# Kernel optimization log

Measured on AMD Instinct MI355X. Metric: run time of the kernel, lower is better.

## Reference

```python
import jax, jax.numpy as jnp
import numpy as np

B, N_OCR, N_OBJ, D, H, L, DFF = 64, 64, 192, 768, 12, 4, 2048
DH = D // H
EPS = 1e-5  # torch LayerNorm default


def _ln(x, g, b):
    m = jnp.mean(x, axis=-1, keepdims=True)
    v = jnp.mean(jnp.square(x - m), axis=-1, keepdims=True)
    return (x - m) * jax.lax.rsqrt(v + EPS) * g + b


def setup_inputs():
    key = jax.random.key(0)
    ks = iter(jax.random.split(key, 32))
    s = 0.02
    f = lambda shape: jax.random.normal(next(ks), shape, jnp.float32) * s
    return {
        "ocr_feats": jax.random.normal(next(ks), (B, N_OCR, D), jnp.float32),
        "obj_feats": jax.random.normal(next(ks), (B, N_OBJ, D), jnp.float32),
        "ocr_dvs": jax.random.uniform(next(ks), (B, N_OCR, 1), jnp.float32, 0.1, 2.0),
        "obj_dvs": jax.random.uniform(next(ks), (B, N_OBJ, 1), jnp.float32, 0.1, 2.0),
        # SemanticAttentionDeFUM projections
        "sa_wq": f((D, D)), "sa_bq": jnp.zeros((D,), jnp.float32),
        "sa_wk": f((D, D)), "sa_bk": jnp.zeros((D,), jnp.float32),
        "sa_wv": f((D, D)), "sa_bv": jnp.zeros((D,), jnp.float32),
        # outer LayerNorm
        "ln0_g": jnp.ones((D,), jnp.float32), "ln0_b": jnp.zeros((D,), jnp.float32),
        # stacked TransformerEncoder layer params (post-norm, batch_first)
        "qkv_w": f((L, 3 * D, D)), "qkv_b": jnp.zeros((L, 3 * D), jnp.float32),
        "out_w": f((L, D, D)), "out_b": jnp.zeros((L, D), jnp.float32),
        "ln1_g": jnp.ones((L, D), jnp.float32), "ln1_b": jnp.zeros((L, D), jnp.float32),
        "ff1_w": f((L, DFF, D)), "ff1_b": jnp.zeros((L, DFF), jnp.float32),
        "ff2_w": f((L, D, DFF)), "ff2_b": jnp.zeros((L, D), jnp.float32),
        "ln2_g": jnp.ones((L, D), jnp.float32), "ln2_b": jnp.zeros((L, D), jnp.float32),
    }


def reference(ocr_feats, obj_feats, ocr_dvs, obj_dvs,
              sa_wq, sa_bq, sa_wk, sa_bk, sa_wv, sa_bv,
              ln0_g, ln0_b,
              qkv_w, qkv_b, out_w, out_b, ln1_g, ln1_b,
              ff1_w, ff1_b, ff2_w, ff2_b, ln2_g, ln2_b):
    num_ocr = ocr_feats.shape[1]
    x = jnp.concatenate([ocr_feats, obj_feats], axis=1)       # B,N,D
    dv = jnp.concatenate([ocr_dvs, obj_dvs], axis=1)[..., 0]  # B,N
    # vectorized cal_relative_depth_map: log(max(dv_i,dv_j)/min(dv_i,dv_j))
    R = jnp.log(jnp.maximum(dv[:, :, None], dv[:, None, :]) /
                jnp.minimum(dv[:, :, None], dv[:, None, :]))  # B,N,N
    # semantic attention: scores A and values V
    q = jnp.einsum('bnd,ed->bne', x, sa_wq) + sa_bq
    k = jnp.einsum('bnd,ed->bne', x, sa_wk) + sa_bk
    v = jnp.einsum('bnd,ed->bne', x, sa_wv) + sa_bv
    A = jnp.einsum('bqd,bkd->bqk', q, k) / jnp.sqrt(jnp.float32(D))
    att = jax.nn.softmax(A + R, axis=-1)
    h = _ln(x + jnp.einsum('bqk,bkd->bqd', att, v), ln0_g, ln0_b)

    def layer(h, p):
        qw, qb, ow, ob, l1g, l1b, f1w, f1b, f2w, f2b, l2g, l2b = p
        Bn, N, _ = h.shape
        qkv = jnp.einsum('bnd,ed->bne', h, qw) + qb            # B,N,3D
        qh, kh, vh = jnp.split(qkv, 3, axis=-1)
        qh = qh.reshape(Bn, N, H, DH).transpose(0, 2, 1, 3)
        kh = kh.reshape(Bn, N, H, DH).transpose(0, 2, 1, 3)
        vh = vh.reshape(Bn, N, H, DH).transpose(0, 2, 1, 3)
        sc = jnp.einsum('bhqd,bhkd->bhqk', qh, kh) / jnp.sqrt(jnp.float32(DH))
        o = jnp.einsum('bhqk,bhkd->bhqd', jax.nn.softmax(sc, axis=-1), vh)
        o = o.transpose(0, 2, 1, 3).reshape(Bn, N, D)
        o = jnp.einsum('bnd,ed->bne', o, ow) + ob
        h = _ln(h + o, l1g, l1b)
        ff = jnp.einsum('bnd,fd->bnf', h, f1w) + f1b
        ff = jax.nn.gelu(ff, approximate=False)  # torch 'gelu' = exact erf gelu
        ff = jnp.einsum('bnf,df->bnd', ff, f2w) + f2b
        h = _ln(h + ff, l2g, l2b)
        return h, None

    h, _ = jax.lax.scan(layer, h, (qkv_w, qkv_b, out_w, out_b,
                                   ln1_g, ln1_b, ff1_w, ff1_b,
                                   ff2_w, ff2_b, ln2_g, ln2_b))
    return h[:, :num_ocr, :]
```

## Files before the change

kernel.cpp:

```cpp
#include <hip/hip_runtime.h>

typedef unsigned short u16;
typedef __bf16 bf16_t;
typedef bf16_t bf16x8 __attribute__((ext_vector_type(8)));
typedef float f32x4 __attribute__((ext_vector_type(4)));
typedef unsigned int u32x4 __attribute__((ext_vector_type(4)));
typedef u16 u16x4 __attribute__((ext_vector_type(4)));

#define GL_LDS16(gp, lp)                                              \
  __builtin_amdgcn_global_load_lds(                                   \
      (const __attribute__((address_space(1))) void*)(gp),            \
      (__attribute__((address_space(3))) void*)(lp), 16, 0, 0)

__device__ __forceinline__ u16 f2bf(float f) {
  unsigned u = __builtin_bit_cast(unsigned, f);
  u += 0x7fff + ((u >> 16) & 1);
  return (u16)(u >> 16);
}
__device__ __forceinline__ float bf2f(u16 h) {
  unsigned u = ((unsigned)h) << 16;
  return __builtin_bit_cast(float, u);
}
__device__ __forceinline__ float wredSum(float v) {
#pragma unroll
  for (int m = 32; m; m >>= 1) v += __shfl_xor(v, m);
  return v;
}

__global__ __launch_bounds__(256, 2) void gemm3r(
    const u16* __restrict__ A, const u16* __restrict__ B,
    const float* __restrict__ bias, u16* __restrict__ C,
    int K, int N, int gx, int act, int tstore) {
  extern __shared__ __align__(16) char sm[];
  const int tid = threadIdx.x;
  const int l = tid & 63, wc = tid >> 6, lg = l >> 4, li = l & 15;

  int bid = blockIdx.x;
  int G = gx >> 3;
  int xcd = bid & 7, loc = bid >> 3;
  int mt = xcd * G + (loc % G), nt = loc / G;

  const u16* Ab = A + (long)mt * 128 * K;
  const u16* Bb = B + (long)nt * 256 * K;

  const long saoff = (long)(tid >> 2) * K + (((tid & 3) ^ ((tid >> 3) & 3)) << 3);
  const long rowK64 = (long)64 * K;
  const int t16 = tid * 16;

#define STAGE(bi_, kt_)                                                \
  do {                                                                 \
    char* lb_ = sm + (bi_) * 24576;                                    \
    const u16* gb_ = Bb + saoff + ((long)(kt_) << 5);                  \
    GL_LDS16(gb_, lb_ + 8192 + t16);                                   \
    GL_LDS16(gb_ + rowK64, lb_ + 12288 + t16);                         \
    GL_LDS16(gb_ + 2 * rowK64, lb_ + 16384 + t16);                     \
    GL_LDS16(gb_ + 3 * rowK64, lb_ + 20480 + t16);                     \
    const u16* ga_ = Ab + saoff + ((long)(kt_) << 5);                  \
    GL_LDS16(ga_, lb_ + t16);                                          \
    GL_LDS16(ga_ + rowK64, lb_ + 4096 + t16);                          \
  } while (0)

#define VM6 asm volatile("s_waitcnt vmcnt(6)" ::: "memory")
#define VM0 asm volatile("s_waitcnt vmcnt(0)" ::: "memory")

  int aof[2][4], bof[4];
#pragma unroll
  for (int hi = 0; hi < 2; ++hi)
#pragma unroll
    for (int f = 0; f < 4; ++f) {
      int ra = hi * 64 + f * 16 + li;
      aof[hi][f] = ra * 64 + ((lg ^ ((ra >> 1) & 3)) << 4);
    }
#pragma unroll
  for (int f = 0; f < 4; ++f) {
    int rb = wc * 64 + f * 16 + li;
    bof[f] = 8192 + rb * 64 + ((lg ^ ((rb >> 1) & 3)) << 4);
  }

  f32x4 acc[8][4] = {};

  const int NT = K >> 5;
  STAGE(0, 0); STAGE(1, 1);

  for (int s = 0; s < NT; ++s) {
    const int bi = s % 3;
    const char* ab = sm + bi * 24576;
    if (s == NT - 1) VM0; else VM6;
    __builtin_amdgcn_s_barrier();
    asm volatile("" ::: "memory");
    if (s + 2 < NT) { int b2 = (s + 2) % 3; STAGE(b2, s + 2); }
    bf16x8 afr[4], bfr[4], ag[4];
#pragma unroll
    for (int f = 0; f < 4; ++f) {
      afr[f] = __builtin_bit_cast(bf16x8, *(const u32x4*)(ab + aof[0][f]));
      bfr[f] = __builtin_bit_cast(bf16x8, *(const u32x4*)(ab + bof[f]));
      ag[f]  = __builtin_bit_cast(bf16x8, *(const u32x4*)(ab + aof[1][f]));
    }
    __builtin_amdgcn_s_setprio(1);
#pragma unroll
    for (int fi = 0; fi < 4; ++fi)
#pragma unroll
      for (int fj = 0; fj < 4; ++fj)
        acc[fi][fj] = __builtin_amdgcn_mfma_f32_16x16x32_bf16(afr[fi], bfr[fj], acc[fi][fj], 0, 0, 0);
#pragma unroll
    for (int fi = 0; fi < 4; ++fi)
#pragma unroll
      for (int fj = 0; fj < 4; ++fj)
        acc[4 + fi][fj] = __builtin_amdgcn_mfma_f32_16x16x32_bf16(ag[fi], bfr[fj], acc[4 + fi][fj], 0, 0, 0);
    __builtin_amdgcn_s_setprio(0);
  }

  long row0 = (long)mt * 128;
  int col0 = nt * 256 + wc * 64;
#pragma unroll
  for (int fi = 0; fi < 8; ++fi) {
#pragma unroll
    for (int fj = 0; fj < 4; ++fj) {
      int c = col0 + fj * 16 + li;
      float bv = bias ? bias[c] : 0.f;
#pragma unroll
      for (int r = 0; r < 4; ++r) {
        float v = acc[fi][fj][r] + bv;
        if (act) v = 0.5f * v * (1.f + erff(v * 0.70710678118f));
        long row = row0 + fi * 16 + lg * 4 + r;
        long idx = tstore ? ((row >> 8) * 196608 + (long)c * 256 + (row & 255))
                          : (row * (long)N + c);
        C[idx] = f2bf(v);
      }
    }
  }
#undef STAGE
#undef VM6
#undef VM0
}

__global__ __launch_bounds__(256) void gemm_bt(
    const u16* __restrict__ A, const u16* __restrict__ B,
    const float* __restrict__ bias, const float* __restrict__ logdv,
    float* __restrict__ Cf, u16* __restrict__ Cb,
    int K, int ldc, long sA, long sB, long sC, float alpha, int act, int tstore) {
  __shared__ __align__(16) u16 As[2][128 * 32];
  __shared__ __align__(16) u16 Bs[2][128 * 32];
  int tid = threadIdx.x, w = tid >> 6, l = tid & 63, lg = l >> 4, li = l & 15;
  int wr = w >> 1, wc = w & 1;
  long bz = blockIdx.z;
  const u16* Ab = A + bz * sA + (long)blockIdx.x * 128 * K;
  const u16* Bb = B + bz * sB + (long)blockIdx.y * 128 * K;

  int sr = tid >> 2, ss = tid & 3;
  long ga0 = (long)sr * K + ((ss ^ ((sr >> 1) & 3)) << 3);
  long gstep = (long)K << 6;

  int aoff[4], boff[4];
#pragma unroll
  for (int i = 0; i < 4; ++i) {
    int ra = wr * 64 + i * 16 + li;
    aoff[i] = ra * 64 + ((lg ^ ((ra >> 1) & 3)) << 4);
    int rb = wc * 64 + i * 16 + li;
    boff[i] = rb * 64 + ((lg ^ ((rb >> 1) & 3)) << 4);
  }

  f32x4 acc[4][4] = {};
  int wb = w * 1024;

  GL_LDS16(Ab + ga0, (char*)As + wb);
  GL_LDS16(Ab + ga0 + gstep, (char*)As + 4096 + wb);
  GL_LDS16(Bb + ga0, (char*)Bs + wb);
  GL_LDS16(Bb + ga0 + gstep, (char*)Bs + 4096 + wb);
  __syncthreads();

  int T = K >> 5;
  int bsel = 0;
  for (int kt = 0; kt < T; ++kt) {
    if (kt + 1 < T) {
      long ko = (long)(kt + 1) << 5;
      char* an = (char*)As + (bsel ^ 1) * 8192;
      char* bn = (char*)Bs + (bsel ^ 1) * 8192;
      GL_LDS16(Ab + ga0 + ko, an + wb);
      GL_LDS16(Ab + ga0 + gstep + ko, an + 4096 + wb);
      GL_LDS16(Bb + ga0 + ko, bn + wb);
      GL_LDS16(Bb + ga0 + gstep + ko, bn + 4096 + wb);
    }
    char* ac = (char*)As + bsel * 8192;
    char* bc = (char*)Bs + bsel * 8192;
    bf16x8 af[4], bq[4];
#pragma unroll
    for (int i = 0; i < 4; ++i) {
      af[i] = __builtin_bit_cast(bf16x8, *(const u32x4*)(ac + aoff[i]));
      bq[i] = __builtin_bit_cast(bf16x8, *(const u32x4*)(bc + boff[i]));
    }
#pragma unroll
    for (int i = 0; i < 4; ++i)
#pragma unroll
      for (int j = 0; j < 4; ++j)
        acc[i][j] = __builtin_amdgcn_mfma_f32_16x16x32_bf16(af[i], bq[j], acc[i][j], 0, 0, 0);
    __syncthreads();
    bsel ^= 1;
  }

  long row0 = (long)blockIdx.x * 128 + wr * 64;
  int col0 = blockIdx.y * 128 + wc * 64;
  float* cf = Cf ? Cf + bz * sC : (float*)0;
  u16* cb = Cb ? Cb + bz * sC : (u16*)0;
  const float* ldv = logdv ? logdv + bz * 256 : (const float*)0;
#pragma unroll
  for (int i = 0; i < 4; ++i) {
    long rb0 = row0 + i * 16 + lg * 4;
#pragma unroll
    for (int j = 0; j < 4; ++j) {
      int c = col0 + j * 16 + li;
      float bv = bias ? bias[c] : 0.f;
      float lj = ldv ? ldv[c] : 0.f;
#pragma unroll
      for (int r = 0; r < 4; ++r) {
        float v = acc[i][j][r] * alpha + bv;
        if (ldv) v += fabsf(ldv[rb0 + r] - lj);
        if (act) v = 0.5f * v * (1.f + erff(v * 0.70710678118f));
        long row = rb0 + r;
        long idx = tstore ? ((row >> 8) * 196608 + (long)c * 256 + (row & 255))
                          : (row * ldc + c);
        if (cf) cf[idx] = v;
        if (cb) cb[idx] = f2bf(v);
      }
    }
  }
}

__global__ __launch_bounds__(256) void mha_k(const u16* __restrict__ qkv, u16* __restrict__ obf) {
  __shared__ __align__(16) u16 Ks[256 * 64];
  __shared__ __align__(16) u16 Vt[64 * 256];
  int b = blockIdx.y;
  int h = blockIdx.x >> 2, qt = blockIdx.x & 3;
  int tid = threadIdx.x, w = tid >> 6, l = tid & 63, lg = l >> 4, li = l & 15;
  const u16* kb_ = qkv + (long)b * 256 * 2304 + 768 + h * 64;
  const u16* vb_ = qkv + (long)b * 256 * 2304 + 1536 + h * 64;
#pragma unroll
  for (int it = 0; it < 8; ++it) {
    int c = it * 256 + tid; int n = c >> 3, sl = c & 7;
    u32x4 d = *(const u32x4*)(kb_ + (long)n * 2304 + sl * 8);
    *(u32x4*)((char*)Ks + n * 128 + ((sl ^ (n & 7)) << 4)) = d;
  }
#pragma unroll
  for (int it = 0; it < 8; ++it) {
    int c = it * 256 + tid; int n = c >> 3, sl = c & 7;
    u32x4 dv = *(const u32x4*)(vb_ + (long)n * 2304 + sl * 8);
    const u16* pe = (const u16*)&dv;
#pragma unroll
    for (int j = 0; j < 8; ++j) {
      int dd = sl * 8 + j;
      *(u16*)((char*)Vt + dd * 512 + (((n >> 3) ^ (dd & 7)) << 4) + (n & 7) * 2) = pe[j];
    }
  }
  __syncthreads();

  long qrow = (long)b * 256 + qt * 64 + w * 16 + li;
  const u16* qp = qkv + qrow * 2304 + h * 64;
  bf16x8 qf0 = __builtin_bit_cast(bf16x8, *(const u32x4*)(qp + lg * 8));
  bf16x8 qf1 = __builtin_bit_cast(bf16x8, *(const u32x4*)(qp + 32 + lg * 8));

  f32x4 sacc[16] = {};
#pragma unroll
  for (int jt = 0; jt < 16; ++jt) {
    int j = jt * 16 + li;
    u32x4 k0 = *(const u32x4*)((char*)Ks + j * 128 + ((lg ^ (j & 7)) << 4));
    u32x4 k1 = *(const u32x4*)((char*)Ks + j * 128 + (((4 + lg) ^ (j & 7)) << 4));
    sacc[jt] = __builtin_amdgcn_mfma_f32_16x16x32_bf16(qf0, __builtin_bit_cast(bf16x8, k0), sacc[jt], 0, 0, 0);
    sacc[jt] = __builtin_amdgcn_mfma_f32_16x16x32_bf16(qf1, __builtin_bit_cast(bf16x8, k1), sacc[jt], 0, 0, 0);
  }
#pragma unroll
  for (int jt = 0; jt < 16; ++jt) sacc[jt] = sacc[jt] * 0.125f;

  float rinv[4];
#pragma unroll
  for (int r = 0; r < 4; ++r) {
    float m = -1e30f;
#pragma unroll
    for (int jt = 0; jt < 16; ++jt) m = fmaxf(m, sacc[jt][r]);
#pragma unroll
    for (int mk = 1; mk < 16; mk <<= 1) m = fmaxf(m, __shfl_xor(m, mk));
    float s = 0.f;
#pragma unroll
    for (int jt = 0; jt < 16; ++jt) { float e = __expf(sacc[jt][r] - m); sacc[jt][r] = e; s += e; }
#pragma unroll
    for (int mk = 1; mk < 16; mk <<= 1) s += __shfl_xor(s, mk);
    rinv[r] = 1.f / s;
  }
  __syncthreads();
  char* Ps = (char*)Ks + w * 8192;
#pragma unroll
  for (int jt = 0; jt < 16; ++jt) {
    int j = jt * 16 + li;
#pragma unroll
    for (int r = 0; r < 4; ++r) {
      int i = lg * 4 + r;
      *(u16*)(Ps + i * 512 + (((j >> 3) ^ (i & 7)) << 4) + (j & 7) * 2) = f2bf(sacc[jt][r]);
    }
  }
  __syncthreads();
  f32x4 oacc[4] = {};
#pragma unroll
  for (int kb2 = 0; kb2 < 8; ++kb2) {
    int sl = kb2 * 4 + lg;
    u32x4 pa = *(const u32x4*)(Ps + li * 512 + ((sl ^ (li & 7)) << 4));
#pragma unroll
    for (int dt = 0; dt < 4; ++dt) {
      int dd = dt * 16 + li;
      u32x4 vv = *(const u32x4*)((char*)Vt + dd * 512 + ((sl ^ (dd & 7)) << 4));
      oacc[dt] = __builtin_amdgcn_mfma_f32_16x16x32_bf16(__builtin_bit_cast(bf16x8, pa),
                                                         __builtin_bit_cast(bf16x8, vv), oacc[dt], 0, 0, 0);
    }
  }
  long orow = (long)b * 256 + qt * 64 + w * 16;
#pragma unroll
  for (int dt = 0; dt < 4; ++dt)
#pragma unroll
    for (int r = 0; r < 4; ++r) {
      float vvv = oacc[dt][r] * rinv[r];
      obf[(orow + lg * 4 + r) * 768 + h * 64 + dt * 16 + li] = f2bf(vvv);
    }
}

__global__ __launch_bounds__(256) void ln_k(const float* __restrict__ X, const u16* __restrict__ Rr,
                                            const float* __restrict__ g, const float* __restrict__ bb,
                                            float* __restrict__ oF, u16* __restrict__ oB) {
  long row = (long)blockIdx.x * 4 + (threadIdx.x >> 6);
  int l = threadIdx.x & 63;
  const float* x = X + row * 768;
  const u16* rr = Rr + row * 768;
  f32x4 v[3];
  float s = 0.f;
#pragma unroll
  for (int i = 0; i < 3; ++i) {
    f32x4 xv = *(const f32x4*)(x + i * 256 + l * 4);
    u16x4 rv = *(const u16x4*)(rr + i * 256 + l * 4);
#pragma unroll
    for (int j = 0; j < 4; ++j) xv[j] += bf2f(rv[j]);
    v[i] = xv;
    s += xv[0] + xv[1] + xv[2] + xv[3];
  }
  float mean = wredSum(s) * (1.f / 768.f);
  float q = 0.f;
#pragma unroll
  for (int i = 0; i < 3; ++i) {
#pragma unroll
    for (int j = 0; j < 4; ++j) { v[i][j] -= mean; q += v[i][j] * v[i][j]; }
  }
  float inv = rsqrtf(wredSum(q) * (1.f / 768.f) + 1e-5f);
#pragma unroll
  for (int i = 0; i < 3; ++i) {
    f32x4 gv = *(const f32x4*)(g + i * 256 + l * 4);
    f32x4 bv = *(const f32x4*)(bb + i * 256 + l * 4);
    f32x4 o;
    u16x4 ob;
#pragma unroll
    for (int j = 0; j < 4; ++j) { o[j] = v[i][j] * inv * gv[j] + bv[j]; ob[j] = f2bf(o[j]); }
    *(f32x4*)(oF + row * 768 + i * 256 + l * 4) = o;
    *(u16x4*)(oB + row * 768 + i * 256 + l * 4) = ob;
  }
}

__global__ __launch_bounds__(256) void smax_k(const float* __restrict__ S, u16* __restrict__ P) {
  long row = (long)blockIdx.x * 4 + (threadIdx.x >> 6);
  int l = threadIdx.x & 63;
  f32x4 v = *(const f32x4*)(S + row * 256 + l * 4);
  float m = fmaxf(fmaxf(v[0], v[1]), fmaxf(v[2], v[3]));
#pragma unroll
  for (int mk = 1; mk < 64; mk <<= 1) m = fmaxf(m, __shfl_xor(m, mk));
  float e0 = __expf(v[0] - m), e1 = __expf(v[1] - m), e2 = __expf(v[2] - m), e3 = __expf(v[3] - m);
  float s = wredSum(e0 + e1 + e2 + e3);
  float rn = 1.f / s;
  u16x4 o; o[0] = f2bf(e0 * rn); o[1] = f2bf(e1 * rn); o[2] = f2bf(e2 * rn); o[3] = f2bf(e3 * rn);
  *(u16x4*)(P + row * 256 + l * 4) = o;
}

__global__ __launch_bounds__(256) void conv_k(const float* __restrict__ in, u16* __restrict__ out, long n4) {
  long i = (long)blockIdx.x * 256 + threadIdx.x;
  if (i >= n4) return;
  f32x4 v = *(const f32x4*)(in + i * 4);
  u16x4 o; o[0] = f2bf(v[0]); o[1] = f2bf(v[1]); o[2] = f2bf(v[2]); o[3] = f2bf(v[3]);
  *(u16x4*)(out + i * 4) = o;
}

__global__ __launch_bounds__(256) void concat_k(const float* __restrict__ ocr, const float* __restrict__ obj,
                                                float* __restrict__ xf, u16* __restrict__ xb) {
  long i = (long)blockIdx.x * 256 + threadIdx.x;
  if (i >= 16384L * 192) return;
  long row = i / 192; int c4 = (int)(i % 192);
  int b = (int)(row >> 8), n = (int)(row & 255);
  const float* src = (n < 64) ? (ocr + ((long)(b * 64 + n)) * 768) : (obj + ((long)(b * 192 + n - 64)) * 768);
  f32x4 v = *(const f32x4*)(src + c4 * 4);
  *(f32x4*)(xf + row * 768 + c4 * 4) = v;
  u16x4 o; o[0] = f2bf(v[0]); o[1] = f2bf(v[1]); o[2] = f2bf(v[2]); o[3] = f2bf(v[3]);
  *(u16x4*)(xb + row * 768 + c4 * 4) = o;
}

__global__ __launch_bounds__(256) void logdv_k(const float* __restrict__ ocr_dv, const float* __restrict__ obj_dv,
                                               float* __restrict__ out) {
  int i = blockIdx.x * 256 + threadIdx.x;
  if (i >= 16384) return;
  int b = i >> 8, n = i & 255;
  float dv = (n < 64) ? ocr_dv[b * 64 + n] : obj_dv[b * 192 + n - 64];
  out[i] = logf(dv);
}

__global__ __launch_bounds__(256) void slice_k(const float* __restrict__ H, float* __restrict__ O) {
  long i = (long)blockIdx.x * 256 + threadIdx.x;
  if (i >= 786432) return;
  long idx = i * 4;
  long row = idx / 768; int c = (int)(idx % 768);
  long b = row >> 6, n = row & 63;
  *(f32x4*)(O + idx) = *(const f32x4*)(H + ((b * 256 + n) * 768 + c));
}

extern "C" void kernel_launch(void* const* d_in, const int* in_sizes, int n_in,
                              void* d_out, int out_size, void* d_ws, size_t ws_size,
                              hipStream_t stream) {
  const float* ocr = (const float*)d_in[0];
  const float* obj = (const float*)d_in[1];
  const float* ocr_dv = (const float*)d_in[2];
  const float* obj_dv = (const float*)d_in[3];
  const float* sa_wq = (const float*)d_in[4];
  const float* sa_bq = (const float*)d_in[5];
  const float* sa_wk = (const float*)d_in[6];
  const float* sa_bk = (const float*)d_in[7];
  const float* sa_wv = (const float*)d_in[8];
  const float* sa_bv = (const float*)d_in[9];
  const float* ln0_g = (const float*)d_in[10];
  const float* ln0_b = (const float*)d_in[11];
  const float* qkv_w = (const float*)d_in[12];
  const float* qkv_b = (const float*)d_in[13];
  const float* out_w = (const float*)d_in[14];
  const float* out_b = (const float*)d_in[15];
  const float* ln1_g = (const float*)d_in[16];
  const float* ln1_b = (const float*)d_in[17];
  const float* ff1_w = (const float*)d_in[18];
  const float* ff1_b = (const float*)d_in[19];
  const float* ff2_w = (const float*)d_in[20];
  const float* ff2_b = (const float*)d_in[21];
  const float* ln2_g = (const float*)d_in[22];
  const float* ln2_b = (const float*)d_in[23];

  (void)hipFuncSetAttribute((const void*)gemm3r,
                            hipFuncAttributeMaxDynamicSharedMemorySize, 73728);
  const unsigned DSM = 73728;

  char* ws = (char*)d_ws;
  float* XF = (float*)ws;
  u16* HB = (u16*)(ws + 50331648);
  float* LDV = (float*)(ws + 75497472);
  u16* WCV = (u16*)(ws + 75563008);
  char* SCR = ws + 86573056;

  const int bigws = ws_size >= (size_t)187236352;

  auto cv = [&](const float* src, long elems, u16* dst) {
    long n4 = elems >> 2;
    conv_k<<<dim3((unsigned)((n4 + 255) / 256)), dim3(256), 0, stream>>>(src, dst, n4);
  };

  concat_k<<<12288, 256, 0, stream>>>(ocr, obj, XF, HB);
  logdv_k<<<64, 256, 0, stream>>>(ocr_dv, obj_dv, LDV);

  const float SSC = 0.03608439182435161f;

  cv(sa_wq, 589824, WCV);
  cv(sa_wk, 589824, WCV + 589824);
  cv(sa_wv, 589824, WCV + 1179648);

  if (bigws) {
    u16* Qf = (u16*)SCR;
    u16* Kf = (u16*)(SCR + 25165824);
    u16* VTf = (u16*)(SCR + 50331648);
    float* Sfc = (float*)(SCR + 75497472);
    u16* Pc = (u16*)(SCR + 83886080);
    u16* ATTc = (u16*)(SCR + 88080384);
    gemm3r<<<384, 256, DSM, stream>>>(HB, WCV, sa_bq, Qf, 768, 768, 128, 0, 0);
    gemm3r<<<384, 256, DSM, stream>>>(HB, WCV + 589824, sa_bk, Kf, 768, 768, 128, 0, 0);
    gemm3r<<<384, 256, DSM, stream>>>(HB, WCV + 1179648, sa_bv, VTf, 768, 768, 128, 0, 1);
    for (int c = 0; c < 2; ++c) {
      long base = (long)c * 8192;
      gemm_bt<<<dim3(2, 2, 32), 256, 0, stream>>>(Qf + base * 768, Kf + base * 768, nullptr,
                                                  LDV + c * 8192, Sfc, nullptr, 768, 256,
                                                  196608, 196608, 65536, SSC, 0, 0);
      smax_k<<<2048, 256, 0, stream>>>(Sfc, Pc);
      gemm_bt<<<dim3(2, 6, 32), 256, 0, stream>>>(Pc, VTf + base * 768, nullptr, nullptr,
                                                  nullptr, ATTc, 256, 768, 65536, 196608, 196608, 1.f, 0, 0);
      ln_k<<<2048, 256, 0, stream>>>(XF + base * 768, ATTc, ln0_g, ln0_b, XF + base * 768, HB + base * 768);
    }
    u16* QKVf = (u16*)SCR;
    u16* Of = (u16*)(SCR + 75497472);
    u16* PRf = (u16*)SCR;
    u16* FFf = (u16*)(SCR + 25165824);
    for (int l = 0; l < 4; ++l) {
      cv(qkv_w + (long)l * 1769472, 1769472, WCV);
      cv(out_w + (long)l * 589824, 589824, WCV + 1769472);
      cv(ff1_w + (long)l * 1572864, 1572864, WCV + 2359296);
      cv(ff2_w + (long)l * 1572864, 1572864, WCV + 3932160);
      gemm3r<<<1152, 256, DSM, stream>>>(HB, WCV, qkv_b + l * 2304, QKVf, 768, 2304, 128, 0, 0);
      mha_k<<<dim3(48, 64), 256, 0, stream>>>(QKVf, Of);
      gemm3r<<<384, 256, DSM, stream>>>(Of, WCV + 1769472, out_b + l * 768, PRf, 768, 768, 128, 0, 0);
      ln_k<<<4096, 256, 0, stream>>>(XF, PRf, ln1_g + l * 768, ln1_b + l * 768, XF, HB);
      gemm3r<<<1024, 256, DSM, stream>>>(HB, WCV + 2359296, ff1_b + l * 2048, FFf, 768, 2048, 128, 1, 0);
      gemm3r<<<384, 256, DSM, stream>>>(FFf, WCV + 3932160, ff2_b + l * 768, PRf, 2048, 768, 128, 0, 0);
      ln_k<<<4096, 256, 0, stream>>>(XF, PRf, ln2_g + l * 768, ln2_b + l * 768, XF, HB);
    }
  } else {
    for (int c = 0; c < 2; ++c) {
      long base = (long)c * 8192;
      u16* Qc = (u16*)SCR;
      u16* Kc = (u16*)(SCR + 12582912);
      u16* VTc = (u16*)(SCR + 25165824);
      float* Sfc = (float*)(SCR + 37748736);
      u16* Pc = (u16*)(SCR + 46137344);
      u16* ATTc = (u16*)(SCR + 50331648);
      gemm3r<<<192, 256, DSM, stream>>>(HB + base * 768, WCV, sa_bq, Qc, 768, 768, 64, 0, 0);
      gemm3r<<<192, 256, DSM, stream>>>(HB + base * 768, WCV + 589824, sa_bk, Kc, 768, 768, 64, 0, 0);
      gemm3r<<<192, 256, DSM, stream>>>(HB + base * 768, WCV + 1179648, sa_bv, VTc, 768, 768, 64, 0, 1);
      gemm_bt<<<dim3(2, 2, 32), 256, 0, stream>>>(Qc, Kc, nullptr, LDV + c * 8192,
                                                  Sfc, nullptr, 768, 256, 196608, 196608, 65536, SSC, 0, 0);
      smax_k<<<2048, 256, 0, stream>>>(Sfc, Pc);
      gemm_bt<<<dim3(2, 6, 32), 256, 0, stream>>>(Pc, VTc, nullptr, nullptr,
                                                  nullptr, ATTc, 256, 768, 65536, 196608, 196608, 1.f, 0, 0);
      ln_k<<<2048, 256, 0, stream>>>(XF + base * 768, ATTc, ln0_g, ln0_b, XF + base * 768, HB + base * 768);
    }
    for (int l = 0; l < 4; ++l) {
      cv(qkv_w + (long)l * 1769472, 1769472, WCV);
      cv(out_w + (long)l * 589824, 589824, WCV + 1769472);
      cv(ff1_w + (long)l * 1572864, 1572864, WCV + 2359296);
      cv(ff2_w + (long)l * 1572864, 1572864, WCV + 3932160);
      for (int c = 0; c < 2; ++c) {
        long base = (long)c * 8192;
        u16* QKVc = (u16*)SCR;
        u16* Oc = (u16*)(SCR + 37748736);
        u16* PRc = (u16*)(SCR + 50331648);
        u16* FFc = (u16*)SCR;
        gemm3r<<<576, 256, DSM, stream>>>(HB + base * 768, WCV, qkv_b + l * 2304, QKVc, 768, 2304, 64, 0, 0);
        mha_k<<<dim3(48, 32), 256, 0, stream>>>(QKVc, Oc);
        gemm3r<<<192, 256, DSM, stream>>>(Oc, WCV + 1769472, out_b + l * 768, PRc, 768, 768, 64, 0, 0);
        ln_k<<<2048, 256, 0, stream>>>(XF + base * 768, PRc, ln1_g + l * 768, ln1_b + l * 768,
                                       XF + base * 768, HB + base * 768);
        gemm3r<<<512, 256, DSM, stream>>>(HB + base * 768, WCV + 2359296, ff1_b + l * 2048, FFc, 768, 2048, 64, 1, 0);
        gemm3r<<<192, 256, DSM, stream>>>(FFc, WCV + 3932160, ff2_b + l * 768, PRc, 2048, 768, 64, 0, 0);
        ln_k<<<2048, 256, 0, stream>>>(XF + base * 768, PRc, ln2_g + l * 768, ln2_b + l * 768,
                                       XF + base * 768, HB + base * 768);
      }
    }
  }
  slice_k<<<3072, 256, 0, stream>>>(XF, (float*)d_out);
}
```

Baseline: 1.952 ms.

## Make GEMM persistent with cross-tile prefetch and drop fp32 residual stream

```diff
diff --git a/kernel.cpp b/kernel.cpp
--- a/kernel.cpp
+++ b/kernel.cpp
@@ -27,35 +27,31 @@
   return v;
 }
 
-__global__ __launch_bounds__(256, 2) void gemm3r(
+__global__ __launch_bounds__(256, 2) void gemmp(
     const u16* __restrict__ A, const u16* __restrict__ B,
     const float* __restrict__ bias, u16* __restrict__ C,
-    int K, int N, int gx, int act, int tstore) {
+    int K, int N, int gx, int gy, int act, int tstore) {
   extern __shared__ __align__(16) char sm[];
   const int tid = threadIdx.x;
-  const int l = tid & 63, wc = tid >> 6, lg = l >> 4, li = l & 15;
-
-  int bid = blockIdx.x;
-  int G = gx >> 3;
-  int xcd = bid & 7, loc = bid >> 3;
-  int mt = xcd * G + (loc % G), nt = loc / G;
-
-  const u16* Ab = A + (long)mt * 128 * K;
-  const u16* Bb = B + (long)nt * 256 * K;
-
+  const int l = tid & 63, wv = tid >> 6, lg = l >> 4, li = l & 15;
+  const int TOT = gx * gy;
+  int tix = blockIdx.x;
+  if (tix >= TOT) return;
+  const int G = gx >> 3;
+
+  const long rowK64 = (long)64 * K;
   const long saoff = (long)(tid >> 2) * K + (((tid & 3) ^ ((tid >> 3) & 3)) << 3);
-  const long rowK64 = (long)64 * K;
   const int t16 = tid * 16;
 
-#define STAGE(bi_, kt_)                                                \
+#define STAGE(bi_, Ap_, Bp_, kt_)                                      \
   do {                                                                 \
     char* lb_ = sm + (bi_) * 24576;                                    \
-    const u16* gb_ = Bb + saoff + ((long)(kt_) << 5);                  \
+    const u16* gb_ = (Bp_) + saoff + ((long)(kt_) << 5);               \
     GL_LDS16(gb_, lb_ + 8192 + t16);                                   \
     GL_LDS16(gb_ + rowK64, lb_ + 12288 + t16);                         \
     GL_LDS16(gb_ + 2 * rowK64, lb_ + 16384 + t16);                     \
     GL_LDS16(gb_ + 3 * rowK64, lb_ + 20480 + t16);                     \
-    const u16* ga_ = Ab + saoff + ((long)(kt_) << 5);                  \
+    const u16* ga_ = (Ap_) + saoff + ((long)(kt_) << 5);               \
     GL_LDS16(ga_, lb_ + t16);                                          \
     GL_LDS16(ga_ + rowK64, lb_ + 4096 + t16);                          \
   } while (0)
@@ -73,61 +69,87 @@
     }
 #pragma unroll
   for (int f = 0; f < 4; ++f) {
-    int rb = wc * 64 + f * 16 + li;
+    int rb = wv * 64 + f * 16 + li;
     bof[f] = 8192 + rb * 64 + ((lg ^ ((rb >> 1) & 3)) << 4);
   }
 
+  int mt, nt;
+  const u16 *cA, *cB;
+  { int xc = tix & 7, lo = tix >> 3;
+    mt = xc * G + lo % G; nt = lo / G;
+    cA = A + (long)mt * 128 * K; cB = B + (long)nt * 256 * K; }
+  int nxt = tix + 512;
+  int hasn = nxt < TOT;
+  int nmt = 0, nnt = 0;
+  const u16 *nA = cA, *nB = cB;
+  if (hasn) { int xc = nxt & 7, lo = nxt >> 3;
+    nmt = xc * G + lo % G; nnt = lo / G;
+    nA = A + (long)nmt * 128 * K; nB = B + (long)nnt * 256 * K; }
+
+  const int NT = K >> 5;
   f32x4 acc[8][4] = {};
-
-  const int NT = K >> 5;
-  STAGE(0, 0); STAGE(1, 1);
-
-  for (int s = 0; s < NT; ++s) {
-    const int bi = s % 3;
-    const char* ab = sm + bi * 24576;
-    if (s == NT - 1) VM0; else VM6;
-    __builtin_amdgcn_s_barrier();
-    asm volatile("" ::: "memory");
-    if (s + 2 < NT) { int b2 = (s + 2) % 3; STAGE(b2, s + 2); }
-    bf16x8 afr[4], bfr[4], ag[4];
-#pragma unroll
-    for (int f = 0; f < 4; ++f) {
-      afr[f] = __builtin_bit_cast(bf16x8, *(const u32x4*)(ab + aof[0][f]));
-      bfr[f] = __builtin_bit_cast(bf16x8, *(const u32x4*)(ab + bof[f]));
-      ag[f]  = __builtin_bit_cast(bf16x8, *(const u32x4*)(ab + aof[1][f]));
-    }
-    __builtin_amdgcn_s_setprio(1);
-#pragma unroll
-    for (int fi = 0; fi < 4; ++fi)
-#pragma unroll
-      for (int fj = 0; fj < 4; ++fj)
-        acc[fi][fj] = __builtin_amdgcn_mfma_f32_16x16x32_bf16(afr[fi], bfr[fj], acc[fi][fj], 0, 0, 0);
-#pragma unroll
-    for (int fi = 0; fi < 4; ++fi)
-#pragma unroll
-      for (int fj = 0; fj < 4; ++fj)
-        acc[4 + fi][fj] = __builtin_amdgcn_mfma_f32_16x16x32_bf16(ag[fi], bfr[fj], acc[4 + fi][fj], 0, 0, 0);
-    __builtin_amdgcn_s_setprio(0);
-  }
-
-  long row0 = (long)mt * 128;
-  int col0 = nt * 256 + wc * 64;
-#pragma unroll
-  for (int fi = 0; fi < 8; ++fi) {
-#pragma unroll
-    for (int fj = 0; fj < 4; ++fj) {
-      int c = col0 + fj * 16 + li;
-      float bv = bias ? bias[c] : 0.f;
-#pragma unroll
-      for (int r = 0; r < 4; ++r) {
-        float v = acc[fi][fj][r] + bv;
-        if (act) v = 0.5f * v * (1.f + erff(v * 0.70710678118f));
-        long row = row0 + fi * 16 + lg * 4 + r;
-        long idx = tstore ? ((row >> 8) * 196608 + (long)c * 256 + (row & 255))
-                          : (row * (long)N + c);
-        C[idx] = f2bf(v);
+  STAGE(0, cA, cB, 0); STAGE(1, cA, cB, 1);
+  int bi = 0;
+
+  for (;;) {
+    for (int s = 0; s < NT; ++s) {
+      int bi2 = bi + 2; if (bi2 >= 3) bi2 -= 3;
+      const char* ab = sm + bi * 24576;
+      if (s == NT - 1 && !hasn) VM0; else VM6;
+      __builtin_amdgcn_s_barrier();
+      asm volatile("" ::: "memory");
+      int s2 = s + 2;
+      if (s2 < NT) STAGE(bi2, cA, cB, s2);
+      else if (hasn) STAGE(bi2, nA, nB, s2 - NT);
+      bf16x8 afr[4], bfr[4], ag[4];
+#pragma unroll
+      for (int f = 0; f < 4; ++f) {
+        afr[f] = __builtin_bit_cast(bf16x8, *(const u32x4*)(ab + aof[0][f]));
+        bfr[f] = __builtin_bit_cast(bf16x8, *(const u32x4*)(ab + bof[f]));
+        ag[f]  = __builtin_bit_cast(bf16x8, *(const u32x4*)(ab + aof[1][f]));
       }
-    }
+      __builtin_amdgcn_s_setprio(1);
+#pragma unroll
+      for (int fi = 0; fi < 4; ++fi)
+#pragma unroll
+        for (int fj = 0; fj < 4; ++fj)
+          acc[fi][fj] = __builtin_amdgcn_mfma_f32_16x16x32_bf16(afr[fi], bfr[fj], acc[fi][fj], 0, 0, 0);
+#pragma unroll
+      for (int fi = 0; fi < 4; ++fi)
+#pragma unroll
+        for (int fj = 0; fj < 4; ++fj)
+          acc[4 + fi][fj] = __builtin_amdgcn_mfma_f32_16x16x32_bf16(ag[fi], bfr[fj], acc[4 + fi][fj], 0, 0, 0);
+      __builtin_amdgcn_s_setprio(0);
+      bi = bi + 1; if (bi == 3) bi = 0;
+    }
+    {
+      long row0 = (long)mt * 128;
+      int col0 = nt * 256 + wv * 64;
+#pragma unroll
+      for (int fi = 0; fi < 8; ++fi) {
+#pragma unroll
+        for (int fj = 0; fj < 4; ++fj) {
+          int c = col0 + fj * 16 + li;
+          float bv = bias ? bias[c] : 0.f;
+#pragma unroll
+          for (int r = 0; r < 4; ++r) {
+            float v = acc[fi][fj][r] + bv;
+            if (act) v = 0.5f * v * (1.f + erff(v * 0.70710678118f));
+            long row = row0 + fi * 16 + lg * 4 + r;
+            long idx = tstore ? ((row >> 8) * 196608 + (long)c * 256 + (row & 255))
+                              : (row * (long)N + c);
+            C[idx] = f2bf(v);
+          }
+          acc[fi][fj] = (f32x4){0.f, 0.f, 0.f, 0.f};
+        }
+      }
+    }
+    if (!hasn) break;
+    mt = nmt; nt = nnt; cA = nA; cB = nB;
+    tix = nxt; nxt += 512; hasn = nxt < TOT;
+    if (hasn) { int xc = nxt & 7, lo = nxt >> 3;
+      nmt = xc * G + lo % G; nnt = lo / G;
+      nA = A + (long)nmt * 128 * K; nB = B + (long)nnt * 256 * K; }
   }
 #undef STAGE
 #undef VM6
@@ -320,23 +342,24 @@
     }
 }
 
-__global__ __launch_bounds__(256) void ln_k(const float* __restrict__ X, const u16* __restrict__ Rr,
+__global__ __launch_bounds__(256) void ln_k(const u16* __restrict__ X, const u16* __restrict__ Rr,
                                             const float* __restrict__ g, const float* __restrict__ bb,
-                                            float* __restrict__ oF, u16* __restrict__ oB) {
+                                            u16* __restrict__ O) {
   long row = (long)blockIdx.x * 4 + (threadIdx.x >> 6);
   int l = threadIdx.x & 63;
-  const float* x = X + row * 768;
+  const u16* x = X + row * 768;
   const u16* rr = Rr + row * 768;
   f32x4 v[3];
   float s = 0.f;
 #pragma unroll
   for (int i = 0; i < 3; ++i) {
-    f32x4 xv = *(const f32x4*)(x + i * 256 + l * 4);
+    u16x4 xv = *(const u16x4*)(x + i * 256 + l * 4);
     u16x4 rv = *(const u16x4*)(rr + i * 256 + l * 4);
-#pragma unroll
-    for (int j = 0; j < 4; ++j) xv[j] += bf2f(rv[j]);
-    v[i] = xv;
-    s += xv[0] + xv[1] + xv[2] + xv[3];
+    f32x4 t;
+#pragma unroll
+    for (int j = 0; j < 4; ++j) t[j] = bf2f(xv[j]) + bf2f(rv[j]);
+    v[i] = t;
+    s += t[0] + t[1] + t[2] + t[3];
   }
   float mean = wredSum(s) * (1.f / 768.f);
   float q = 0.f;
@@ -350,12 +373,10 @@
   for (int i = 0; i < 3; ++i) {
     f32x4 gv = *(const f32x4*)(g + i * 256 + l * 4);
     f32x4 bv = *(const f32x4*)(bb + i * 256 + l * 4);
-    f32x4 o;
     u16x4 ob;
 #pragma unroll
-    for (int j = 0; j < 4; ++j) { o[j] = v[i][j] * inv * gv[j] + bv[j]; ob[j] = f2bf(o[j]); }
-    *(f32x4*)(oF + row * 768 + i * 256 + l * 4) = o;
-    *(u16x4*)(oB + row * 768 + i * 256 + l * 4) = ob;
+    for (int j = 0; j < 4; ++j) ob[j] = f2bf(v[i][j] * inv * gv[j] + bv[j]);
+    *(u16x4*)(O + row * 768 + i * 256 + l * 4) = ob;
   }
 }
 
@@ -382,14 +403,13 @@
 }
 
 __global__ __launch_bounds__(256) void concat_k(const float* __restrict__ ocr, const float* __restrict__ obj,
-                                                float* __restrict__ xf, u16* __restrict__ xb) {
+                                                u16* __restrict__ xb) {
   long i = (long)blockIdx.x * 256 + threadIdx.x;
   if (i >= 16384L * 192) return;
   long row = i / 192; int c4 = (int)(i % 192);
   int b = (int)(row >> 8), n = (int)(row & 255);
   const float* src = (n < 64) ? (ocr + ((long)(b * 64 + n)) * 768) : (obj + ((long)(b * 192 + n - 64)) * 768);
   f32x4 v = *(const f32x4*)(src + c4 * 4);
-  *(f32x4*)(xf + row * 768 + c4 * 4) = v;
   u16x4 o; o[0] = f2bf(v[0]); o[1] = f2bf(v[1]); o[2] = f2bf(v[2]); o[3] = f2bf(v[3]);
   *(u16x4*)(xb + row * 768 + c4 * 4) = o;
 }
@@ -403,13 +423,15 @@
   out[i] = logf(dv);
 }
 
-__global__ __launch_bounds__(256) void slice_k(const float* __restrict__ H, float* __restrict__ O) {
+__global__ __launch_bounds__(256) void slice_k(const u16* __restrict__ H, float* __restrict__ O) {
   long i = (long)blockIdx.x * 256 + threadIdx.x;
   if (i >= 786432) return;
   long idx = i * 4;
   long row = idx / 768; int c = (int)(idx % 768);
   long b = row >> 6, n = row & 63;
-  *(f32x4*)(O + idx) = *(const f32x4*)(H + ((b * 256 + n) * 768 + c));
+  u16x4 v = *(const u16x4*)(H + ((b * 256 + n) * 768 + c));
+  f32x4 o; o[0] = bf2f(v[0]); o[1] = bf2f(v[1]); o[2] = bf2f(v[2]); o[3] = bf2f(v[3]);
+  *(f32x4*)(O + idx) = o;
 }
 
 extern "C" void kernel_launch(void* const* d_in, const int* in_sizes, int n_in,
@@ -440,25 +462,24 @@
   const float* ln2_g = (const float*)d_in[22];
   const float* ln2_b = (const float*)d_in[23];
 
-  (void)hipFuncSetAttribute((const void*)gemm3r,
+  (void)hipFuncSetAttribute((const void*)gemmp,
                             hipFuncAttributeMaxDynamicSharedMemorySize, 73728);
   const unsigned DSM = 73728;
 
   char* ws = (char*)d_ws;
-  float* XF = (float*)ws;
-  u16* HB = (u16*)(ws + 50331648);
-  float* LDV = (float*)(ws + 75497472);
-  u16* WCV = (u16*)(ws + 75563008);
-  char* SCR = ws + 86573056;
-
-  const int bigws = ws_size >= (size_t)187236352;
+  u16* HB = (u16*)ws;
+  float* LDV = (float*)(ws + 25165824);
+  u16* WCV = (u16*)(ws + 25231360);
+  char* SCR = ws + 36241408;
+
+  const int bigws = ws_size >= (size_t)137953280;
 
   auto cv = [&](const float* src, long elems, u16* dst) {
     long n4 = elems >> 2;
     conv_k<<<dim3((unsigned)((n4 + 255) / 256)), dim3(256), 0, stream>>>(src, dst, n4);
   };
 
-  concat_k<<<12288, 256, 0, stream>>>(ocr, obj, XF, HB);
+  concat_k<<<12288, 256, 0, stream>>>(ocr, obj, HB);
   logdv_k<<<64, 256, 0, stream>>>(ocr_dv, obj_dv, LDV);
 
   const float SSC = 0.03608439182435161f;
@@ -474,9 +495,9 @@
     float* Sfc = (float*)(SCR + 75497472);
     u16* Pc = (u16*)(SCR + 83886080);
     u16* ATTc = (u16*)(SCR + 88080384);
-    gemm3r<<<384, 256, DSM, stream>>>(HB, WCV, sa_bq, Qf, 768, 768, 128, 0, 0);
-    gemm3r<<<384, 256, DSM, stream>>>(HB, WCV + 589824, sa_bk, Kf, 768, 768, 128, 0, 0);
-    gemm3r<<<384, 256, DSM, stream>>>(HB, WCV + 1179648, sa_bv, VTf, 768, 768, 128, 0, 1);
+    gemmp<<<512, 256, DSM, stream>>>(HB, WCV, sa_bq, Qf, 768, 768, 128, 3, 0, 0);
+    gemmp<<<512, 256, DSM, stream>>>(HB, WCV + 589824, sa_bk, Kf, 768, 768, 128, 3, 0, 0);
+    gemmp<<<512, 256, DSM, stream>>>(HB, WCV + 1179648, sa_bv, VTf, 768, 768, 128, 3, 0, 1);
     for (int c = 0; c < 2; ++c) {
       long base = (long)c * 8192;
       gemm_bt<<<dim3(2, 2, 32), 256, 0, stream>>>(Qf + base * 768, Kf + base * 768, nullptr,
@@ -485,7 +506,7 @@
       smax_k<<<2048, 256, 0, stream>>>(Sfc, Pc);
       gemm_bt<<<dim3(2, 6, 32), 256, 0, stream>>>(Pc, VTf + base * 768, nullptr, nullptr,
                                                   nullptr, ATTc, 256, 768, 65536, 196608, 196608, 1.f, 0, 0);
-      ln_k<<<2048, 256, 0, stream>>>(XF + base * 768, ATTc, ln0_g, ln0_b, XF + base * 768, HB + base * 768);
+      ln_k<<<2048, 256, 0, stream>>>(HB + base * 768, ATTc, ln0_g, ln0_b, HB + base * 768);
     }
     u16* QKVf = (u16*)SCR;
     u16* Of = (u16*)(SCR + 75497472);
@@ -496,13 +517,13 @@
       cv(out_w + (long)l * 589824, 589824, WCV + 1769472);
       cv(ff1_w + (long)l * 1572864, 1572864, WCV + 2359296);
       cv(ff2_w + (long)l * 1572864, 1572864, WCV + 3932160);
-      gemm3r<<<1152, 256, DSM, stream>>>(HB, WCV, qkv_b + l * 2304, QKVf, 768, 2304, 128, 0, 0);
+      gemmp<<<512, 256, DSM, stream>>>(HB, WCV, qkv_b + l * 2304, QKVf, 768, 2304, 128, 9, 0, 0);
       mha_k<<<dim3(48, 64), 256, 0, stream>>>(QKVf, Of);
-      gemm3r<<<384, 256, DSM, stream>>>(Of, WCV + 1769472, out_b + l * 768, PRf, 768, 768, 128, 0, 0);
-      ln_k<<<4096, 256, 0, stream>>>(XF, PRf, ln1_g + l * 768, ln1_b + l * 768, XF, HB);
-      gemm3r<<<1024, 256, DSM, stream>>>(HB, WCV + 2359296, ff1_b + l * 2048, FFf, 768, 2048, 128, 1, 0);
-      gemm3r<<<384, 256, DSM, stream>>>(FFf, WCV + 3932160, ff2_b + l * 768, PRf, 2048, 768, 128, 0, 0);
-      ln_k<<<4096, 256, 0, stream>>>(XF, PRf, ln2_g + l * 768, ln2_b + l * 768, XF, HB);
+      gemmp<<<512, 256, DSM, stream>>>(Of, WCV + 1769472, out_b + l * 768, PRf, 768, 768, 128, 3, 0, 0);
+      ln_k<<<4096, 256, 0, stream>>>(HB, PRf, ln1_g + l * 768, ln1_b + l * 768, HB);
+      gemmp<<<512, 256, DSM, stream>>>(HB, WCV + 2359296, ff1_b + l * 2048, FFf, 768, 2048, 128, 8, 1, 0);
+      gemmp<<<512, 256, DSM, stream>>>(FFf, WCV + 3932160, ff2_b + l * 768, PRf, 2048, 768, 128, 3, 0, 0);
+      ln_k<<<4096, 256, 0, stream>>>(HB, PRf, ln2_g + l * 768, ln2_b + l * 768, HB);
     }
   } else {
     for (int c = 0; c < 2; ++c) {
@@ -513,15 +534,15 @@
       float* Sfc = (float*)(SCR + 37748736);
       u16* Pc = (u16*)(SCR + 46137344);
       u16* ATTc = (u16*)(SCR + 50331648);
-      gemm3r<<<192, 256, DSM, stream>>>(HB + base * 768, WCV, sa_bq, Qc, 768, 768, 64, 0, 0);
-      gemm3r<<<192, 256, DSM, stream>>>(HB + base * 768, WCV + 589824, sa_bk, Kc, 768, 768, 64, 0, 0);
-      gemm3r<<<192, 256, DSM, stream>>>(HB + base * 768, WCV + 1179648, sa_bv, VTc, 768, 768, 64, 0, 1);
+      gemmp<<<512, 256, DSM, stream>>>(HB + base * 768, WCV, sa_bq, Qc, 768, 768, 64, 3, 0, 0);
+      gemmp<<<512, 256, DSM, stream>>>(HB + base * 768, WCV + 589824, sa_bk, Kc, 768, 768, 64, 3, 0, 0);
+      gemmp<<<512, 256, DSM, stream>>>(HB + base * 768, WCV + 1179648, sa_bv, VTc, 768, 768, 64, 3, 0, 1);
       gemm_bt<<<dim3(2, 2, 32), 256, 0, stream>>>(Qc, Kc, nullptr, LDV + c * 8192,
                                                   Sfc, nullptr, 768, 256, 196608, 196608, 65536, SSC, 0, 0);
       smax_k<<<2048, 256, 0, stream>>>(Sfc, Pc);
       gemm_bt<<<dim3(2, 6, 32), 256, 0, stream>>>(Pc, VTc, nullptr, nullptr,
                                                   nullptr, ATTc, 256, 768, 65536, 196608, 196608, 1.f, 0, 0);
-      ln_k<<<2048, 256, 0, stream>>>(XF + base * 768, ATTc, ln0_g, ln0_b, XF + base * 768, HB + base * 768);
+      ln_k<<<2048, 256, 0, stream>>>(HB + base * 768, ATTc, ln0_g, ln0_b, HB + base * 768);
     }
     for (int l = 0; l < 4; ++l) {
       cv(qkv_w + (long)l * 1769472, 1769472, WCV);
@@ -534,17 +555,15 @@
         u16* Oc = (u16*)(SCR + 37748736);
         u16* PRc = (u16*)(SCR + 50331648);
         u16* FFc = (u16*)SCR;
-        gemm3r<<<576, 256, DSM, stream>>>(HB + base * 768, WCV, qkv_b + l * 2304, QKVc, 768, 2304, 64, 0, 0);
+        gemmp<<<512, 256, DSM, stream>>>(HB + base * 768, WCV, qkv_b + l * 2304, QKVc, 768, 2304, 64, 9, 0, 0);
         mha_k<<<dim3(48, 32), 256, 0, stream>>>(QKVc, Oc);
-        gemm3r<<<192, 256, DSM, stream>>>(Oc, WCV + 1769472, out_b + l * 768, PRc, 768, 768, 64, 0, 0);
-        ln_k<<<2048, 256, 0, stream>>>(XF + base * 768, PRc, ln1_g + l * 768, ln1_b + l * 768,
-                                       XF + base * 768, HB + base * 768);
-        gemm3r<<<512, 256, DSM, stream>>>(HB + base * 768, WCV + 2359296, ff1_b + l * 2048, FFc, 768, 2048, 64, 1, 0);
-        gemm3r<<<192, 256, DSM, stream>>>(FFc, WCV + 3932160, ff2_b + l * 768, PRc, 2048, 768, 64, 0, 0);
-        ln_k<<<2048, 256, 0, stream>>>(XF + base * 768, PRc, ln2_g + l * 768, ln2_b + l * 768,
-                                       XF + base * 768, HB + base * 768);
+        gemmp<<<512, 256, DSM, stream>>>(Oc, WCV + 1769472, out_b + l * 768, PRc, 768, 768, 64, 3, 0, 0);
+        ln_k<<<2048, 256, 0, stream>>>(HB + base * 768, PRc, ln1_g + l * 768, ln1_b + l * 768, HB + base * 768);
+        gemmp<<<512, 256, DSM, stream>>>(HB + base * 768, WCV + 2359296, ff1_b + l * 2048, FFc, 768, 2048, 64, 8, 1, 0);
+        gemmp<<<512, 256, DSM, stream>>>(FFc, WCV + 3932160, ff2_b + l * 768, PRc, 2048, 768, 64, 3, 0, 0);
+        ln_k<<<2048, 256, 0, stream>>>(HB + base * 768, PRc, ln2_g + l * 768, ln2_b + l * 768, HB + base * 768);
       }
     }
   }
-  slice_k<<<3072, 256, 0, stream>>>(XF, (float*)d_out);
-}
+  slice_k<<<3072, 256, 0, stream>>>(HB, (float*)d_out);
+}
```

Result: faster. 1.843 ms (-5.6%).
